# Optimization experiments

Measured on AMD Instinct MI355X. Metric: run time of the kernel, lower is better.

Reference implementation:

```python
import jax, jax.numpy as jnp
import numpy as np

K = 16
ITERS = 5
DIST_CHUNK = 8  # feature-chunk size to avoid materializing [B,F,S,S]


def pairwise_l1(x):
    """x: [B, F, S] -> d: [B, S, S], d[b,i,j] = ||x[b,:,i]-x[b,:,j]||_1.
    Computed in feature chunks via scan so peak intermediate is [B,CH,S,S]."""
    B, F, S = x.shape
    xc = x.reshape(B, F // DIST_CHUNK, DIST_CHUNK, S).transpose(1, 0, 2, 3)  # [F/CH,B,CH,S]

    def step(acc, blk):  # blk: [B, CH, S]
        return acc + jnp.abs(blk[:, :, :, None] - blk[:, :, None, :]).sum(axis=1), None

    d, _ = jax.lax.scan(step, jnp.zeros((B, S, S), x.dtype), xc)
    return d


def kmedoids_pool(x, w):
    B, F, S = x.shape
    wm = jnp.mean(w, axis=1)                       # [B,S] per-token attention weight
    d = pairwise_l1(x)                             # [B,S,S]
    _, ctr = jax.lax.top_k(wm, K)                  # [B,K] initial medoids
    dw = d * wm[:, None, :]                        # d[b,i,j]*w[b,j]
    for _ in range(ITERS):
        # distance from every token to each current medoid: [B,S,K]
        i2c = jnp.take_along_axis(d, jnp.broadcast_to(ctr[:, None, :], (B, S, K)), axis=2)
        assign = jnp.argmin(i2c, axis=2)           # [B,S] cluster assignment
        member = jax.nn.one_hot(assign, K, dtype=x.dtype)  # [B,S,K]
        # weighted within-cluster cost for candidate i in cluster k:
        # cost[b,i,k] = sum_j d[b,i,j]*w[b,j]*member[b,j,k]
        cost = jnp.einsum('bij,bjk->bik', dw, member)
        cost = jnp.where(member > 0, cost, jnp.inf)  # medoid must be a member
        ctr = jnp.argmin(cost, axis=1)             # [B,K] new medoids
    idx = jnp.broadcast_to(ctr[:, None, :], (B, F, K))
    return jnp.take_along_axis(x, idx, axis=2)     # [B,F,K]


def setup_inputs() -> dict:
    key = jax.random.key(0)
    kx, kw = jax.random.split(key)
    B, F, S = 8, 256, 1024
    x = jax.random.normal(kx, (B, F, S), dtype=jnp.float32)
    w = jax.random.uniform(kw, (B, S, S), dtype=jnp.float32)
    return {"x": x, "w": w}


def reference(x, w):
    return kmedoids_pool(x, w)
```

## Files before the change

kernel.cpp:

```cpp
#include <hip/hip_runtime.h>
#include <math.h>

#define BB 8
#define FF 256
#define SS 1024
#define KK 16
#define ITERS 5

#define ICH 8
__global__ void wm_part_kernel(const float* __restrict__ w, float* __restrict__ part) {
    int j = blockIdx.x * 256 + threadIdx.x;
    int ic = blockIdx.y, b = blockIdx.z;
    const float* wp = w + (size_t)b * SS * SS + (size_t)ic * (SS / ICH) * SS + j;
    float s = 0.f;
#pragma unroll 8
    for (int i = 0; i < SS / ICH; ++i) s += wp[(size_t)i * SS];
    part[((size_t)ic * BB + b) * SS + j] = s;
}

__global__ void wm_final_kernel(const float* __restrict__ part, float* __restrict__ wm) {
    int t = blockIdx.x * blockDim.x + threadIdx.x;
    if (t >= BB * SS) return;
    int b = t / SS, j = t % SS;
    float s = 0.f;
#pragma unroll
    for (int ic = 0; ic < ICH; ++ic) s += part[((size_t)ic * BB + b) * SS + j];
    wm[t] = s * (1.0f / SS);
}

#define TS 64
#define FC 16
__global__ __launch_bounds__(256) void dist_kernel(const float* __restrict__ x,
                                                   float* __restrict__ d) {
    __shared__ float smbuf[TS * (TS + 1)];
    float (*As)[TS] = reinterpret_cast<float(*)[TS]>(smbuf);
    float (*Bs)[TS] = reinterpret_cast<float(*)[TS]>(smbuf + FC * TS);
    float (*tr)[TS + 1] = reinterpret_cast<float(*)[TS + 1]>(smbuf);

    int b = blockIdx.y;
    int t = blockIdx.x;
    int it = 0;
    while (t >= (SS / TS) - it) { t -= (SS / TS) - it; ++it; }
    int jt = it + t;
    int i0 = it * TS;
    int j0 = jt * TS;

    int tid = threadIdx.x;
    int tx = tid & 15, ty = tid >> 4;
    const float* xb = x + (size_t)b * FF * SS;
    float* db = d + (size_t)b * SS * SS;
    float acc[4][4] = {};
    for (int f0 = 0; f0 < FF; f0 += FC) {
#pragma unroll
        for (int r = 0; r < 4; ++r) {
            int l = tid + r * 256;
            int f = l >> 6, tok = l & 63;
            As[f][tok] = xb[(size_t)(f0 + f) * SS + i0 + tok];
            Bs[f][tok] = xb[(size_t)(f0 + f) * SS + j0 + tok];
        }
        __syncthreads();
#pragma unroll
        for (int f = 0; f < FC; ++f) {
            float4 a = *(const float4*)&As[f][ty * 4];
            float4 bb = *(const float4*)&Bs[f][tx * 4];
            float av[4] = {a.x, a.y, a.z, a.w};
            float bv[4] = {bb.x, bb.y, bb.z, bb.w};
#pragma unroll
            for (int r = 0; r < 4; ++r)
#pragma unroll
                for (int c = 0; c < 4; ++c)
                    acc[r][c] += fabsf(av[r] - bv[c]);
        }
        __syncthreads();
    }
#pragma unroll
    for (int r = 0; r < 4; ++r) {
        float4 v = make_float4(acc[r][0], acc[r][1], acc[r][2], acc[r][3]);
        *(float4*)&db[(size_t)(i0 + ty * 4 + r) * SS + j0 + tx * 4] = v;
    }
    if (jt != it) {
#pragma unroll
        for (int r = 0; r < 4; ++r)
#pragma unroll
            for (int c = 0; c < 4; ++c)
                tr[tx * 4 + c][ty * 4 + r] = acc[r][c];
        __syncthreads();
#pragma unroll
        for (int q = 0; q < 4; ++q) {
            int row = q * 16 + (tid >> 4);
            int col = (tid & 15) * 4;
            float4 v;
            v.x = tr[row][col];
            v.y = tr[row][col + 1];
            v.z = tr[row][col + 2];
            v.w = tr[row][col + 3];
            *(float4*)&db[(size_t)(j0 + row) * SS + i0 + col] = v;
        }
    }
}

__global__ void topk_kernel(const float* __restrict__ wm, int* __restrict__ ctr) {
    int b = blockIdx.x;
    __shared__ float vals[SS];
    __shared__ float rv[256];
    __shared__ int ri[256];
    int tid = threadIdx.x;
    for (int j = tid; j < SS; j += 256) vals[j] = wm[b * SS + j];
    __syncthreads();
    for (int k = 0; k < KK; ++k) {
        float bv = -INFINITY;
        int bi = 0x7fffffff;
        for (int j = tid; j < SS; j += 256) {
            float v = vals[j];
            if (v > bv) { bv = v; bi = j; }
        }
        rv[tid] = bv; ri[tid] = bi;
        __syncthreads();
        for (int s = 128; s > 0; s >>= 1) {
            if (tid < s) {
                if (rv[tid + s] > rv[tid] ||
                    (rv[tid + s] == rv[tid] && ri[tid + s] < ri[tid])) {
                    rv[tid] = rv[tid + s];
                    ri[tid] = ri[tid + s];
                }
            }
            __syncthreads();
        }
        if (tid == 0) {
            ctr[b * KK + k] = ri[0];
            vals[ri[0]] = -INFINITY;
        }
        __syncthreads();
    }
}

__global__ void assign_kernel(const float* __restrict__ d, const int* __restrict__ ctr,
                              int* __restrict__ assign) {
    int t = blockIdx.x * blockDim.x + threadIdx.x;
    if (t >= BB * SS) return;
    int b = t / SS, i = t % SS;
    const float* db = d + (size_t)b * SS * SS;
    const int* cb = ctr + b * KK;
    float bv = INFINITY;
    int bk = 0;
#pragma unroll
    for (int k = 0; k < KK; ++k) {
        float v = db[(size_t)cb[k] * SS + i];
        if (v < bv) { bv = v; bk = k; }
    }
    assign[t] = bk;
}

__global__ __launch_bounds__(256) void cost_kernel(const float* __restrict__ d,
                                                   const float* __restrict__ wm,
                                                   const int* __restrict__ assign,
                                                   float* __restrict__ cost) {
    int b = blockIdx.y;
    int i = blockIdx.x;
    int tid = threadIdx.x;
    int my = assign[b * SS + i];
    const float* drow = d + (size_t)b * SS * SS + (size_t)i * SS;
    const float* wb = wm + b * SS;
    const int* ab = assign + b * SS;
    float4 dv = *(const float4*)&drow[tid * 4];
    float4 wv = *(const float4*)&wb[tid * 4];
    int4 av = *(const int4*)&ab[tid * 4];
    float s = 0.f;
    s += (av.x == my) ? dv.x * wv.x : 0.f;
    s += (av.y == my) ? dv.y * wv.y : 0.f;
    s += (av.z == my) ? dv.z * wv.z : 0.f;
    s += (av.w == my) ? dv.w * wv.w : 0.f;
#pragma unroll
    for (int off = 32; off > 0; off >>= 1) s += __shfl_down(s, off, 64);
    __shared__ float ws_s[4];
    if ((tid & 63) == 0) ws_s[tid >> 6] = s;
    __syncthreads();
    if (tid == 0) cost[b * SS + i] = (ws_s[0] + ws_s[1]) + (ws_s[2] + ws_s[3]);
}

__global__ void update_kernel(const float* __restrict__ cost, const int* __restrict__ assign,
                              int* __restrict__ ctr) {
    int b = blockIdx.y, k = blockIdx.x;
    int tid = threadIdx.x;
    __shared__ float rv[256];
    __shared__ int ri[256];
    float bv = INFINITY;
    int bi = 0x7fffffff;
    for (int i = tid; i < SS; i += 256) {
        if (assign[b * SS + i] == k) {
            float v = cost[b * SS + i];
            if (v < bv || (v == bv && i < bi)) { bv = v; bi = i; }
        }
    }
    rv[tid] = bv; ri[tid] = bi;
    __syncthreads();
    for (int s = 128; s > 0; s >>= 1) {
        if (tid < s) {
            if (rv[tid + s] < rv[tid] ||
                (rv[tid + s] == rv[tid] && ri[tid + s] < ri[tid])) {
                rv[tid] = rv[tid + s];
                ri[tid] = ri[tid + s];
            }
        }
        __syncthreads();
    }
    if (tid == 0) ctr[b * KK + k] = (ri[0] == 0x7fffffff) ? 0 : ri[0];
}

__global__ void gather_kernel(const float* __restrict__ x, const int* __restrict__ ctr,
                              float* __restrict__ out) {
    int t = blockIdx.x * blockDim.x + threadIdx.x;
    if (t >= BB * FF * KK) return;
    int b = t / (FF * KK);
    int f = (t / KK) % FF;
    int k = t % KK;
    out[t] = x[(size_t)b * FF * SS + (size_t)f * SS + ctr[b * KK + k]];
}

extern "C" void kernel_launch(void* const* d_in, const int* in_sizes, int n_in,
                              void* d_out, int out_size, void* d_ws, size_t ws_size,
                              hipStream_t stream) {
    const float* x = (const float*)d_in[0];
    const float* w = (const float*)d_in[1];
    float* out = (float*)d_out;

    char* ws = (char*)d_ws;
    float* d = (float*)ws;
    size_t off = (size_t)BB * SS * SS * sizeof(float);
    float* wm = (float*)(ws + off);  off += (size_t)BB * SS * sizeof(float);
    int* ctr = (int*)(ws + off);     off += (size_t)BB * KK * sizeof(int);
    int* assign = (int*)(ws + off);  off += (size_t)BB * SS * sizeof(int);
    float* cost = (float*)(ws + off);
    float* part = (float*)ws;

    wm_part_kernel<<<dim3(SS / 256, ICH, BB), 256, 0, stream>>>(w, part);
    wm_final_kernel<<<(BB * SS + 255) / 256, 256, 0, stream>>>(part, wm);
    dist_kernel<<<dim3(136, BB), 256, 0, stream>>>(x, d);
    topk_kernel<<<BB, 256, 0, stream>>>(wm, ctr);
    for (int itr = 0; itr < ITERS; ++itr) {
        assign_kernel<<<(BB * SS + 255) / 256, 256, 0, stream>>>(d, ctr, assign);
        cost_kernel<<<dim3(SS, BB), 256, 0, stream>>>(d, wm, assign, cost);
        update_kernel<<<dim3(KK, BB), 256, 0, stream>>>(cost, assign, ctr);
    }
    gather_kernel<<<(BB * FF * KK + 255) / 256, 256, 0, stream>>>(x, ctr, out);
}
```

Before: 271.7 us.

## Retile distance kernel with async LDS loads and fuse top-k/assign/update/gather kernels

The pairwise L1 kernel moves to 64-thread blocks computing 8x8 outputs per thread, with 64-feature chunks loaded straight into LDS through global_load_lds. The mirrored tile is written from registers rather than through a shared-memory transpose. Top-k, assignment, medoid update and the final gather are merged into per-batch 1024-thread kernels that use packed 64-bit key shuffle reductions. This removes several launches per iteration, but leaves only 136x8 single-wave blocks for the dominant distance kernel, which risks low occupancy and uncoalesced transposed stores.

```diff
diff --git a/kernel.cpp b/kernel.cpp
--- a/kernel.cpp
+++ b/kernel.cpp
@@ -6,6 +6,8 @@
 #define SS 1024
 #define KK 16
 #define ITERS 5
+
+typedef unsigned long long ull;
 
 #define ICH 8
 __global__ void wm_part_kernel(const float* __restrict__ w, float* __restrict__ part) {
@@ -29,126 +31,121 @@
 }
 
 #define TS 64
-#define FC 16
-__global__ __launch_bounds__(256) void dist_kernel(const float* __restrict__ x,
-                                                   float* __restrict__ d) {
-    __shared__ float smbuf[TS * (TS + 1)];
-    float (*As)[TS] = reinterpret_cast<float(*)[TS]>(smbuf);
-    float (*Bs)[TS] = reinterpret_cast<float(*)[TS]>(smbuf + FC * TS);
-    float (*tr)[TS + 1] = reinterpret_cast<float(*)[TS + 1]>(smbuf);
-
+#define FC 64
+__device__ __forceinline__ void async_copy16(const float* g, const float* s) {
+    __builtin_amdgcn_global_load_lds((const __attribute__((address_space(1))) void*)g,
+                                     (__attribute__((address_space(3))) void*)s, 16, 0, 0);
+}
+
+__global__ __launch_bounds__(64, 2) void dist_kernel(const float* __restrict__ x,
+                                                     float* __restrict__ d) {
+    __shared__ float As[FC * TS];
+    __shared__ float Bs[FC * TS];
     int b = blockIdx.y;
     int t = blockIdx.x;
     int it = 0;
-    while (t >= (SS / TS) - it) { t -= (SS / TS) - it; ++it; }
+    while (t >= 16 - it) { t -= 16 - it; ++it; }
     int jt = it + t;
-    int i0 = it * TS;
-    int j0 = jt * TS;
-
-    int tid = threadIdx.x;
-    int tx = tid & 15, ty = tid >> 4;
+    int i0 = it * TS, j0 = jt * TS;
+    int tid = threadIdx.x;
+    int ty = tid >> 3, tx = tid & 7;
     const float* xb = x + (size_t)b * FF * SS;
     float* db = d + (size_t)b * SS * SS;
-    float acc[4][4] = {};
+
+    float acc[8][8] = {};
+    int fl = tid >> 4;
+    int tk = (tid & 15) * 4;
     for (int f0 = 0; f0 < FF; f0 += FC) {
 #pragma unroll
-        for (int r = 0; r < 4; ++r) {
-            int l = tid + r * 256;
-            int f = l >> 6, tok = l & 63;
-            As[f][tok] = xb[(size_t)(f0 + f) * SS + i0 + tok];
-            Bs[f][tok] = xb[(size_t)(f0 + f) * SS + j0 + tok];
-        }
-        __syncthreads();
-#pragma unroll
+        for (int c = 0; c < FC / 4; ++c) {
+            const float* ga = xb + (size_t)(f0 + c * 4 + fl) * SS + i0 + tk;
+            const float* gb = xb + (size_t)(f0 + c * 4 + fl) * SS + j0 + tk;
+            async_copy16(ga, &As[c * 256]);
+            async_copy16(gb, &Bs[c * 256]);
+        }
+        __syncthreads();
+#pragma unroll 4
         for (int f = 0; f < FC; ++f) {
-            float4 a = *(const float4*)&As[f][ty * 4];
-            float4 bb = *(const float4*)&Bs[f][tx * 4];
-            float av[4] = {a.x, a.y, a.z, a.w};
-            float bv[4] = {bb.x, bb.y, bb.z, bb.w};
-#pragma unroll
-            for (int r = 0; r < 4; ++r)
-#pragma unroll
-                for (int c = 0; c < 4; ++c)
+            const float* af = &As[f * TS + ty * 8];
+            const float* bf = &Bs[f * TS + tx * 8];
+            float4 a0 = *(const float4*)af;
+            float4 a1 = *(const float4*)(af + 4);
+            float4 b0 = *(const float4*)bf;
+            float4 b1 = *(const float4*)(bf + 4);
+            float av[8] = {a0.x, a0.y, a0.z, a0.w, a1.x, a1.y, a1.z, a1.w};
+            float bv[8] = {b0.x, b0.y, b0.z, b0.w, b1.x, b1.y, b1.z, b1.w};
+#pragma unroll
+            for (int r = 0; r < 8; ++r)
+#pragma unroll
+                for (int c = 0; c < 8; ++c)
                     acc[r][c] += fabsf(av[r] - bv[c]);
         }
         __syncthreads();
     }
 #pragma unroll
-    for (int r = 0; r < 4; ++r) {
-        float4 v = make_float4(acc[r][0], acc[r][1], acc[r][2], acc[r][3]);
-        *(float4*)&db[(size_t)(i0 + ty * 4 + r) * SS + j0 + tx * 4] = v;
+    for (int r = 0; r < 8; ++r) {
+        float4 lo = make_float4(acc[r][0], acc[r][1], acc[r][2], acc[r][3]);
+        float4 hi = make_float4(acc[r][4], acc[r][5], acc[r][6], acc[r][7]);
+        float* p = &db[(size_t)(i0 + ty * 8 + r) * SS + j0 + tx * 8];
+        *(float4*)p = lo;
+        *(float4*)(p + 4) = hi;
     }
     if (jt != it) {
 #pragma unroll
-        for (int r = 0; r < 4; ++r)
-#pragma unroll
-            for (int c = 0; c < 4; ++c)
-                tr[tx * 4 + c][ty * 4 + r] = acc[r][c];
-        __syncthreads();
-#pragma unroll
-        for (int q = 0; q < 4; ++q) {
-            int row = q * 16 + (tid >> 4);
-            int col = (tid & 15) * 4;
-            float4 v;
-            v.x = tr[row][col];
-            v.y = tr[row][col + 1];
-            v.z = tr[row][col + 2];
-            v.w = tr[row][col + 3];
-            *(float4*)&db[(size_t)(j0 + row) * SS + i0 + col] = v;
-        }
-    }
-}
-
-__global__ void topk_kernel(const float* __restrict__ wm, int* __restrict__ ctr) {
+        for (int c = 0; c < 8; ++c) {
+            float4 lo = make_float4(acc[0][c], acc[1][c], acc[2][c], acc[3][c]);
+            float4 hi = make_float4(acc[4][c], acc[5][c], acc[6][c], acc[7][c]);
+            float* p = &db[(size_t)(j0 + tx * 8 + c) * SS + i0 + ty * 8];
+            *(float4*)p = lo;
+            *(float4*)(p + 4) = hi;
+        }
+    }
+}
+
+__global__ __launch_bounds__(1024) void topk_assign_kernel(const float* __restrict__ wm,
+                                                           const float* __restrict__ d,
+                                                           int* __restrict__ assign) {
     int b = blockIdx.x;
-    __shared__ float vals[SS];
-    __shared__ float rv[256];
-    __shared__ int ri[256];
-    int tid = threadIdx.x;
-    for (int j = tid; j < SS; j += 256) vals[j] = wm[b * SS + j];
-    __syncthreads();
+    int tid = threadIdx.x;
+    int lane = tid & 63, wv = tid >> 6;
+    __shared__ ull red[16];
+    __shared__ int ctr_s[KK];
+    float v = wm[b * SS + tid];
+    ull key = (((ull)__float_as_uint(v)) << 32) | (ull)(0xFFFFFFFFu - (unsigned)tid);
     for (int k = 0; k < KK; ++k) {
-        float bv = -INFINITY;
-        int bi = 0x7fffffff;
-        for (int j = tid; j < SS; j += 256) {
-            float v = vals[j];
-            if (v > bv) { bv = v; bi = j; }
-        }
-        rv[tid] = bv; ri[tid] = bi;
-        __syncthreads();
-        for (int s = 128; s > 0; s >>= 1) {
-            if (tid < s) {
-                if (rv[tid + s] > rv[tid] ||
-                    (rv[tid + s] == rv[tid] && ri[tid + s] < ri[tid])) {
-                    rv[tid] = rv[tid + s];
-                    ri[tid] = ri[tid + s];
-                }
+        ull kk = key;
+#pragma unroll
+        for (int off = 32; off; off >>= 1) {
+            ull o = __shfl_down(kk, off, 64);
+            if (o > kk) kk = o;
+        }
+        if (lane == 0) red[wv] = kk;
+        __syncthreads();
+        if (wv == 0) {
+            ull k2 = (lane < 16) ? red[lane] : 0ull;
+#pragma unroll
+            for (int off = 8; off; off >>= 1) {
+                ull o = __shfl_down(k2, off, 64);
+                if (o > k2) k2 = o;
             }
-            __syncthreads();
-        }
-        if (tid == 0) {
-            ctr[b * KK + k] = ri[0];
-            vals[ri[0]] = -INFINITY;
-        }
-        __syncthreads();
-    }
-}
-
-__global__ void assign_kernel(const float* __restrict__ d, const int* __restrict__ ctr,
-                              int* __restrict__ assign) {
-    int t = blockIdx.x * blockDim.x + threadIdx.x;
-    if (t >= BB * SS) return;
-    int b = t / SS, i = t % SS;
+            if (lane == 0) red[0] = k2;
+        }
+        __syncthreads();
+        ull W = red[0];
+        int widx = (int)(0xFFFFFFFFu - (unsigned)(W & 0xFFFFFFFFu));
+        if (tid == widx) key = 0;
+        if (tid == 0) ctr_s[k] = widx;
+        __syncthreads();
+    }
     const float* db = d + (size_t)b * SS * SS;
-    const int* cb = ctr + b * KK;
     float bv = INFINITY;
     int bk = 0;
 #pragma unroll
     for (int k = 0; k < KK; ++k) {
-        float v = db[(size_t)cb[k] * SS + i];
-        if (v < bv) { bv = v; bk = k; }
-    }
-    assign[t] = bk;
+        float vv = db[(size_t)ctr_s[k] * SS + tid];
+        if (vv < bv) { bv = vv; bk = k; }
+    }
+    assign[b * SS + tid] = bk;
 }
 
 __global__ __launch_bounds__(256) void cost_kernel(const float* __restrict__ d,
@@ -178,43 +175,51 @@
     if (tid == 0) cost[b * SS + i] = (ws_s[0] + ws_s[1]) + (ws_s[2] + ws_s[3]);
 }
 
-__global__ void update_kernel(const float* __restrict__ cost, const int* __restrict__ assign,
-                              int* __restrict__ ctr) {
-    int b = blockIdx.y, k = blockIdx.x;
-    int tid = threadIdx.x;
-    __shared__ float rv[256];
-    __shared__ int ri[256];
-    float bv = INFINITY;
-    int bi = 0x7fffffff;
-    for (int i = tid; i < SS; i += 256) {
-        if (assign[b * SS + i] == k) {
-            float v = cost[b * SS + i];
-            if (v < bv || (v == bv && i < bi)) { bv = v; bi = i; }
-        }
-    }
-    rv[tid] = bv; ri[tid] = bi;
+__global__ __launch_bounds__(1024) void update_assign_kernel(
+        const float* __restrict__ d, const float* __restrict__ cost,
+        int* __restrict__ assign, const float* __restrict__ x,
+        float* __restrict__ out, int last) {
+    int b = blockIdx.x;
+    int tid = threadIdx.x;
+    int lane = tid & 63, wv = tid >> 6;
+    __shared__ float cost_s[SS];
+    __shared__ int assign_s[SS];
+    __shared__ int ctr_s[KK];
+    cost_s[tid] = cost[b * SS + tid];
+    assign_s[tid] = assign[b * SS + tid];
     __syncthreads();
-    for (int s = 128; s > 0; s >>= 1) {
-        if (tid < s) {
-            if (rv[tid + s] < rv[tid] ||
-                (rv[tid + s] == rv[tid] && ri[tid + s] < ri[tid])) {
-                rv[tid] = rv[tid + s];
-                ri[tid] = ri[tid + s];
-            }
-        }
-        __syncthreads();
-    }
-    if (tid == 0) ctr[b * KK + k] = (ri[0] == 0x7fffffff) ? 0 : ri[0];
-}
-
-__global__ void gather_kernel(const float* __restrict__ x, const int* __restrict__ ctr,
-                              float* __restrict__ out) {
-    int t = blockIdx.x * blockDim.x + threadIdx.x;
-    if (t >= BB * FF * KK) return;
-    int b = t / (FF * KK);
-    int f = (t / KK) % FF;
-    int k = t % KK;
-    out[t] = x[(size_t)b * FF * SS + (size_t)f * SS + ctr[b * KK + k]];
+    ull best = ~0ull;
+    int k = wv;
+    for (int c = 0; c < SS / 64; ++c) {
+        int i = c * 64 + lane;
+        if (assign_s[i] == k) {
+            ull key = (((ull)__float_as_uint(cost_s[i])) << 32) | (unsigned)i;
+            if (key < best) best = key;
+        }
+    }
+#pragma unroll
+    for (int off = 32; off; off >>= 1) {
+        ull o = __shfl_down(best, off, 64);
+        if (o < best) best = o;
+    }
+    if (lane == 0) ctr_s[k] = (best == ~0ull) ? 0 : (int)(best & 0xFFFFFFFFu);
+    __syncthreads();
+    if (!last) {
+        const float* db = d + (size_t)b * SS * SS;
+        float bv = INFINITY;
+        int bk = 0;
+#pragma unroll
+        for (int k2 = 0; k2 < KK; ++k2) {
+            float vv = db[(size_t)ctr_s[k2] * SS + tid];
+            if (vv < bv) { bv = vv; bk = k2; }
+        }
+        assign[b * SS + tid] = bk;
+    } else {
+        for (int e = tid; e < FF * KK; e += 1024) {
+            int f = e / KK, k2 = e % KK;
+            out[((size_t)b * FF + f) * KK + k2] = x[((size_t)b * FF + f) * SS + ctr_s[k2]];
+        }
+    }
 }
 
 extern "C" void kernel_launch(void* const* d_in, const int* in_sizes, int n_in,
@@ -228,19 +233,17 @@
     float* d = (float*)ws;
     size_t off = (size_t)BB * SS * SS * sizeof(float);
     float* wm = (float*)(ws + off);  off += (size_t)BB * SS * sizeof(float);
-    int* ctr = (int*)(ws + off);     off += (size_t)BB * KK * sizeof(int);
     int* assign = (int*)(ws + off);  off += (size_t)BB * SS * sizeof(int);
     float* cost = (float*)(ws + off);
     float* part = (float*)ws;
 
     wm_part_kernel<<<dim3(SS / 256, ICH, BB), 256, 0, stream>>>(w, part);
     wm_final_kernel<<<(BB * SS + 255) / 256, 256, 0, stream>>>(part, wm);
-    dist_kernel<<<dim3(136, BB), 256, 0, stream>>>(x, d);
-    topk_kernel<<<BB, 256, 0, stream>>>(wm, ctr);
+    dist_kernel<<<dim3(136, BB), 64, 0, stream>>>(x, d);
+    topk_assign_kernel<<<BB, 1024, 0, stream>>>(wm, d, assign);
     for (int itr = 0; itr < ITERS; ++itr) {
-        assign_kernel<<<(BB * SS + 255) / 256, 256, 0, stream>>>(d, ctr, assign);
         cost_kernel<<<dim3(SS, BB), 256, 0, stream>>>(d, wm, assign, cost);
-        update_kernel<<<dim3(KK, BB), 256, 0, stream>>>(cost, assign, ctr);
-    }
-    gather_kernel<<<(BB * FF * KK + 255) / 256, 256, 0, stream>>>(x, ctr, out);
-}
+        update_assign_kernel<<<BB, 1024, 0, stream>>>(d, cost, assign, x, out,
+                                                      itr == ITERS - 1 ? 1 : 0);
+    }
+}
```

Result: slower. 332.3 us (+22.3%).
